# Kernel tuning notes

Measured on AMD Instinct MI355X. Metric: run time of the kernel, lower is better.

The kernel has to match this reference:

```python
import jax, jax.numpy as jnp
import numpy as np

NUM_CLASSES = 10
OUTPUT_DIM = 128
HIDDEN_DIM = 64


def setup_inputs() -> dict:
    key = jax.random.key(0)
    k1, k2, k3, k4, k5, k6 = jax.random.split(key, 6)
    B, S, F = 16, 4096, 512
    X_support = jax.random.normal(k1, (B, S, F), dtype=jnp.float32)
    y_support = jax.random.randint(k2, (B, S), 0, NUM_CLASSES, dtype=jnp.int32)
    # MLP params: Linear(6, HIDDEN) -> GELU -> Linear(HIDDEN, OUTPUT)
    w1 = jax.random.normal(k3, (6, HIDDEN_DIM), dtype=jnp.float32) * (1.0 / np.sqrt(6.0))
    b1 = jax.random.normal(k4, (HIDDEN_DIM,), dtype=jnp.float32) * 0.01
    w2 = jax.random.normal(k5, (HIDDEN_DIM, OUTPUT_DIM), dtype=jnp.float32) * (1.0 / np.sqrt(HIDDEN_DIM))
    b2 = jax.random.normal(k6, (OUTPUT_DIM,), dtype=jnp.float32) * 0.01
    return {"X_support": X_support, "y_support": y_support,
            "w1": w1, "b1": b1, "w2": w2, "b2": b2}


def _feature_target_stats(X, y):
    """Vectorized equivalent of FeatureTargetStatsEncoder per-(batch,feature) loops.
    X: [B, S, F] float, y: [B, S] int class labels. Returns stats [B, F, 6]."""
    B, S, F = X.shape
    missing_rate = jnp.isnan(X).astype(X.dtype).mean(axis=1)           # [B, F]
    Xc = jnp.nan_to_num(X, nan=0.0)
    gmean = Xc.mean(axis=1)                                            # [B, F]
    variance = Xc.var(axis=1)                                          # biased (unbiased=False)
    absX = jnp.abs(Xc)
    mean_abs = absX.mean(axis=1)
    max_abs = absX.max(axis=1)
    # unique_ratio: count distinct values per (b, f) via sort + diff
    xs = jnp.sort(Xc, axis=1)
    n_unique = 1.0 + (jnp.diff(xs, axis=1) != 0).astype(Xc.dtype).sum(axis=1)
    unique_ratio = n_unique / S
    # classification target score: between-class variance / overall variance
    onehot = jax.nn.one_hot(y, NUM_CLASSES, dtype=Xc.dtype)            # [B, S, C]
    counts = onehot.sum(axis=1)                                        # [B, C]
    csum = jnp.einsum('bsc,bsf->bcf', onehot, Xc)                      # [B, C, F]
    cmean = csum / jnp.maximum(counts, 1.0)[:, :, None]
    dev2 = (cmean - gmean[:, None, :]) ** 2
    between = (counts[:, :, None] * dev2).sum(axis=1) / jnp.maximum(counts.sum(axis=1), 1.0)[:, None]
    target_score = between / jnp.maximum(variance, 1e-6)
    stats = jnp.stack([target_score, missing_rate, unique_ratio,
                       variance, mean_abs, max_abs], axis=-1)          # [B, F, 6]
    return jnp.nan_to_num(stats, nan=0.0, posinf=0.0, neginf=0.0)


def reference(X_support, y_support, w1, b1, w2, b2):
    stats = _feature_target_stats(X_support, y_support)                # [B, F, 6]
    h = jax.nn.gelu(stats @ w1 + b1, approximate=False)               # exact GELU like nn.GELU()
    return h @ w2 + b2                                                 # [B, F, OUTPUT_DIM]
```

## Files before the change

### kernel.cpp

```cpp
#include <hip/hip_runtime.h>
#include <math.h>

#define NS 4096
#define NF 512
#define NB 16
#define NC 10
#define HSIZE 8192
#define HMASK 8191
#define HEMPTY 0xFFFFFFFFu
#define WS_XT_OFF 1024

__global__ void count_classes_kernel(const int* __restrict__ y, float* __restrict__ counts) {
    __shared__ int hist[NC];
    const int b = blockIdx.x;
    if (threadIdx.x < NC) hist[threadIdx.x] = 0;
    __syncthreads();
    for (int s = threadIdx.x; s < NS; s += blockDim.x)
        atomicAdd(&hist[y[b * NS + s]], 1);
    __syncthreads();
    if (threadIdx.x < NC) counts[b * NC + threadIdx.x] = (float)hist[threadIdx.x];
}

__device__ __forceinline__ float wave_reduce_add(float v) {
    #pragma unroll
    for (int off = 32; off > 0; off >>= 1) v += __shfl_down(v, off, 64);
    return v;
}
__device__ __forceinline__ float wave_reduce_max(float v) {
    #pragma unroll
    for (int off = 32; off > 0; off >>= 1) v = fmaxf(v, __shfl_down(v, off, 64));
    return v;
}

__launch_bounds__(256)
__global__ void transpose_kernel(const float* __restrict__ X, float* __restrict__ XT,
                                 const int* __restrict__ y, float* __restrict__ counts) {
    __shared__ float t[64][65];
    __shared__ int hist[NC];
    const int b  = blockIdx.x;
    const int s0 = blockIdx.y * 64;
    const int f0 = blockIdx.z * 64;
    const int tid = threadIdx.x;

    const int fi = (tid & 15) * 4;
    const int si = tid >> 4;
    const float* Xb = X + ((size_t)b * NS + s0) * NF + f0;
    #pragma unroll
    for (int i = 0; i < 4; i++) {
        const int s = si + 16 * i;
        const float4 v = *(const float4*)(Xb + (size_t)s * NF + fi);
        t[s][fi + 0] = v.x; t[s][fi + 1] = v.y;
        t[s][fi + 2] = v.z; t[s][fi + 3] = v.w;
    }
    __syncthreads();

    const int sj = (tid & 15) * 4;
    const int fj = tid >> 4;
    float* XTb = XT + ((size_t)b * NF + f0) * NS + s0;
    #pragma unroll
    for (int i = 0; i < 4; i++) {
        const int f = fj + 16 * i;
        float4 v;
        v.x = t[sj + 0][f]; v.y = t[sj + 1][f];
        v.z = t[sj + 2][f]; v.w = t[sj + 3][f];
        *(float4*)(XTb + (size_t)f * NS + sj) = v;
    }

    if (blockIdx.y == 0 && blockIdx.z == 0) {
        if (tid < NC) hist[tid] = 0;
        __syncthreads();
        const int4* yb = (const int4*)(y + (size_t)b * NS);
        #pragma unroll
        for (int i = 0; i < 4; i++) {
            const int4 v = yb[i * 256 + tid];
            atomicAdd(&hist[v.x], 1); atomicAdd(&hist[v.y], 1);
            atomicAdd(&hist[v.z], 1); atomicAdd(&hist[v.w], 1);
        }
        __syncthreads();
        if (tid < NC) counts[b * NC + tid] = (float)hist[tid];
    }
}

__launch_bounds__(512, 8)
__global__ void fused_stats_mlp_xt(const float* __restrict__ XT,
                                   const int* __restrict__ y,
                                   const float* __restrict__ counts,
                                   const float* __restrict__ w1,
                                   const float* __restrict__ b1,
                                   const float* __restrict__ w2,
                                   const float* __restrict__ b2,
                                   float* __restrict__ out) {
    __shared__ __align__(16) unsigned int hash[HSIZE];

    const int w = blockIdx.x;
    const int g = (w & 7) * 1024 + (w >> 3);
    const int b = g >> 9;
    const int f = g & (NF - 1);
    const int tid = threadIdx.x;
    const int wave = tid >> 6, lane = tid & 63;

    uint4* h4 = (uint4*)hash;
    const uint4 e4 = make_uint4(HEMPTY, HEMPTY, HEMPTY, HEMPTY);
    #pragma unroll
    for (int i = 0; i < HSIZE / 4 / 512; i++) h4[i * 512 + tid] = e4;
    __syncthreads();

    const float4* Xc4 = (const float4*)(XT + ((size_t)b * NF + f) * NS);
    const int4*   yp4 = (const int4*)(y + (size_t)b * NS);

    float sum = 0.f, sumsq = 0.f, sumabs = 0.f, maxabs = 0.f, nancnt = 0.f, uniq = 0.f;
    float csum[NC];
    #pragma unroll
    for (int c = 0; c < NC; c++) csum[c] = 0.f;

    float4 xv[2]; int4 yv[2];
    #pragma unroll
    for (int k = 0; k < 2; k++) {
        xv[k] = Xc4[k * 512 + tid];
        yv[k] = yp4[k * 512 + tid];
    }

    #pragma unroll
    for (int k = 0; k < 2; k++) {
        const float xe[4] = { xv[k].x, xv[k].y, xv[k].z, xv[k].w };
        const int   ye[4] = { yv[k].x, yv[k].y, yv[k].z, yv[k].w };
        #pragma unroll
        for (int j = 0; j < 4; j++) {
            float x = xe[j];
            if (x != x) { nancnt += 1.f; x = 0.f; }
            sum += x;
            sumsq = fmaf(x, x, sumsq);
            const float a = fabsf(x);
            sumabs += a;
            maxabs = fmaxf(maxabs, a);
            const int yc = ye[j];
            #pragma unroll
            for (int c = 0; c < NC; c++) csum[c] += (yc == c) ? x : 0.f;
            unsigned int pat = __float_as_uint(x);
            if (pat == 0x80000000u) pat = 0u;
            unsigned int slot = (pat * 2654435761u) >> 19;
            for (;;) {
                const unsigned int old = atomicCAS(&hash[slot], HEMPTY, pat);
                if (old == HEMPTY) { uniq += 1.f; break; }
                if (old == pat) break;
                slot = (slot + 1) & HMASK;
            }
        }
    }

    __syncthreads();

    float (*red)[16] = (float(*)[16])hash;
    float* stats_s   = (float*)hash + 128;
    float* h_s       = (float*)hash + 192;

    sum    = wave_reduce_add(sum);
    sumsq  = wave_reduce_add(sumsq);
    sumabs = wave_reduce_add(sumabs);
    nancnt = wave_reduce_add(nancnt);
    uniq   = wave_reduce_add(uniq);
    maxabs = wave_reduce_max(maxabs);
    #pragma unroll
    for (int c = 0; c < NC; c++) csum[c] = wave_reduce_add(csum[c]);

    if (lane == 0) {
        red[wave][0] = sum;    red[wave][1] = sumsq; red[wave][2] = sumabs;
        red[wave][3] = nancnt; red[wave][4] = uniq;  red[wave][5] = maxabs;
        #pragma unroll
        for (int c = 0; c < NC; c++) red[wave][6 + c] = csum[c];
    }
    __syncthreads();

    if (tid == 0) {
        float t[16];
        #pragma unroll
        for (int v = 0; v < 16; v++) t[v] = red[0][v];
        #pragma unroll
        for (int wv = 1; wv < 8; wv++) {
            #pragma unroll
            for (int v = 0; v < 16; v++) {
                if (v == 5) t[v] = fmaxf(t[v], red[wv][v]);
                else        t[v] += red[wv][v];
            }
        }
        const float invS = 1.f / (float)NS;
        const float gmean    = t[0] * invS;
        const float variance = fmaxf(t[1] * invS - gmean * gmean, 0.f);
        const float mean_abs = t[2] * invS;
        const float missing  = t[3] * invS;
        const float n_unique = t[4];
        const float max_abs  = t[5];
        float between = 0.f;
        #pragma unroll
        for (int c = 0; c < NC; c++) {
            const float cnt = counts[b * NC + c];
            const float cm  = t[6 + c] / fmaxf(cnt, 1.f);
            const float d   = cm - gmean;
            between += cnt * d * d;
        }
        between *= invS;
        const float target = between / fmaxf(variance, 1e-6f);
        float st[6] = { target, missing, n_unique * invS, variance, mean_abs, max_abs };
        #pragma unroll
        for (int i = 0; i < 6; i++) {
            float v = st[i];
            if (!(fabsf(v) < INFINITY)) v = 0.f;
            stats_s[i] = v;
        }
    }
    __syncthreads();

    if (tid < 64) {
        float z = b1[tid];
        #pragma unroll
        for (int i = 0; i < 6; i++) z = fmaf(stats_s[i], w1[i * 64 + tid], z);
        h_s[tid] = 0.5f * z * (1.f + erff(z * 0.70710678118654752440f));
    }
    __syncthreads();
    if (tid < 128) {
        float o = b2[tid];
        #pragma unroll
        for (int j = 0; j < 64; j++) o = fmaf(h_s[j], w2[j * 128 + tid], o);
        out[(size_t)g * 128 + tid] = o;
    }
}

__launch_bounds__(256)
__global__ void fused_stats_mlp_kernel(const float* __restrict__ X,
                                       const int* __restrict__ y,
                                       const float* __restrict__ counts,
                                       const float* __restrict__ w1,
                                       const float* __restrict__ b1,
                                       const float* __restrict__ w2,
                                       const float* __restrict__ b2,
                                       float* __restrict__ out) {
    __shared__ unsigned int hash[HSIZE];
    __shared__ float red[4][16];
    __shared__ float stats_s[6];
    __shared__ float h_s[64];

    const int w = blockIdx.x;
    const int g = (w & 7) * 1024 + (w >> 3);
    const int b = g >> 9;
    const int f = g & (NF - 1);
    const int tid = threadIdx.x;

    #pragma unroll
    for (int i = 0; i < HSIZE / 256; i++) hash[tid + i * 256] = HEMPTY;
    __syncthreads();

    const float* Xp = X + (size_t)b * NS * NF + f;
    const int*   yp = y + b * NS;

    float sum = 0.f, sumsq = 0.f, sumabs = 0.f, maxabs = 0.f, nancnt = 0.f, uniq = 0.f;
    float csum[NC];
    #pragma unroll
    for (int c = 0; c < NC; c++) csum[c] = 0.f;

    #pragma unroll
    for (int k0 = 0; k0 < 16; k0 += 8) {
        float xv[8]; int yv[8];
        #pragma unroll
        for (int k = 0; k < 8; k++) {
            const int s = (k0 + k) * 256 + tid;
            xv[k] = Xp[(size_t)s * NF];
            yv[k] = yp[s];
        }
        #pragma unroll
        for (int k = 0; k < 8; k++) {
            float x = xv[k];
            if (x != x) { nancnt += 1.f; x = 0.f; }
            sum += x;
            sumsq = fmaf(x, x, sumsq);
            const float a = fabsf(x);
            sumabs += a;
            maxabs = fmaxf(maxabs, a);
            const int yc = yv[k];
            #pragma unroll
            for (int c = 0; c < NC; c++) csum[c] += (yc == c) ? x : 0.f;
            unsigned int pat = __float_as_uint(x);
            if (pat == 0x80000000u) pat = 0u;
            unsigned int slot = (pat * 2654435761u) >> 19;
            for (;;) {
                const unsigned int old = atomicCAS(&hash[slot], HEMPTY, pat);
                if (old == HEMPTY) { uniq += 1.f; break; }
                if (old == pat) break;
                slot = (slot + 1) & HMASK;
            }
        }
    }

    sum    = wave_reduce_add(sum);
    sumsq  = wave_reduce_add(sumsq);
    sumabs = wave_reduce_add(sumabs);
    nancnt = wave_reduce_add(nancnt);
    uniq   = wave_reduce_add(uniq);
    maxabs = wave_reduce_max(maxabs);
    #pragma unroll
    for (int c = 0; c < NC; c++) csum[c] = wave_reduce_add(csum[c]);

    const int wave = tid >> 6, lane = tid & 63;
    if (lane == 0) {
        red[wave][0] = sum;    red[wave][1] = sumsq; red[wave][2] = sumabs;
        red[wave][3] = nancnt; red[wave][4] = uniq;  red[wave][5] = maxabs;
        #pragma unroll
        for (int c = 0; c < NC; c++) red[wave][6 + c] = csum[c];
    }
    __syncthreads();

    if (tid == 0) {
        float t[16];
        #pragma unroll
        for (int v = 0; v < 16; v++) t[v] = red[0][v];
        #pragma unroll
        for (int wv = 1; wv < 4; wv++) {
            #pragma unroll
            for (int v = 0; v < 16; v++) {
                if (v == 5) t[v] = fmaxf(t[v], red[wv][v]);
                else        t[v] += red[wv][v];
            }
        }
        const float invS = 1.f / (float)NS;
        const float gmean    = t[0] * invS;
        const float variance = fmaxf(t[1] * invS - gmean * gmean, 0.f);
        const float mean_abs = t[2] * invS;
        const float missing  = t[3] * invS;
        const float n_unique = t[4];
        const float max_abs  = t[5];
        float between = 0.f;
        #pragma unroll
        for (int c = 0; c < NC; c++) {
            const float cnt = counts[b * NC + c];
            const float cm  = t[6 + c] / fmaxf(cnt, 1.f);
            const float d   = cm - gmean;
            between += cnt * d * d;
        }
        between *= invS;
        const float target = between / fmaxf(variance, 1e-6f);
        float st[6] = { target, missing, n_unique * invS, variance, mean_abs, max_abs };
        #pragma unroll
        for (int i = 0; i < 6; i++) {
            float v = st[i];
            if (!(fabsf(v) < INFINITY)) v = 0.f;
            stats_s[i] = v;
        }
    }
    __syncthreads();

    if (tid < 64) {
        float z = b1[tid];
        #pragma unroll
        for (int i = 0; i < 6; i++) z = fmaf(stats_s[i], w1[i * 64 + tid], z);
        h_s[tid] = 0.5f * z * (1.f + erff(z * 0.70710678118654752440f));
    }
    __syncthreads();
    if (tid < 128) {
        float o = b2[tid];
        #pragma unroll
        for (int j = 0; j < 64; j++) o = fmaf(h_s[j], w2[j * 128 + tid], o);
        out[(size_t)g * 128 + tid] = o;
    }
}

extern "C" void kernel_launch(void* const* d_in, const int* in_sizes, int n_in,
                              void* d_out, int out_size, void* d_ws, size_t ws_size,
                              hipStream_t stream) {
    const float* X  = (const float*)d_in[0];
    const int*   y  = (const int*)d_in[1];
    const float* w1 = (const float*)d_in[2];
    const float* b1 = (const float*)d_in[3];
    const float* w2 = (const float*)d_in[4];
    const float* b2 = (const float*)d_in[5];
    float* out    = (float*)d_out;
    float* counts = (float*)d_ws;

    const size_t xt_bytes = (size_t)NB * NF * NS * sizeof(float);
    if (ws_size >= xt_bytes + WS_XT_OFF) {
        float* XT = (float*)((char*)d_ws + WS_XT_OFF);
        transpose_kernel<<<dim3(NB, NS / 64, NF / 64), 256, 0, stream>>>(X, XT, y, counts);
        fused_stats_mlp_xt<<<NB * NF, 512, 0, stream>>>(XT, y, counts, w1, b1, w2, b2, out);
    } else {
        count_classes_kernel<<<NB, 256, 0, stream>>>(y, counts);
        fused_stats_mlp_kernel<<<NB * NF, 256, 0, stream>>>(X, y, counts, w1, b1, w2, b2, out);
    }
}
```

Measured before the change: 388.7 us.

## Split stats and hash-unique work across wave groups with batched CAS

Splits the 512-thread block so waves 0-3 compute moments and class sums over 16 elements each, while waves 4-7 insert the same 16 elements into the shared-memory hash. Hash inserts are batched as 8 independent atomicCAS operations issued before any collision is resolved, so their LDS latency can overlap. The goal is to overlap ALU-heavy reduction with LDS-atomic-heavy unique counting and to raise memory-level parallelism. Each thread now handles twice as many elements, which raises register pressure, and X is loaded twice, by both wave groups.

```diff
diff --git a/kernel.cpp b/kernel.cpp
--- a/kernel.cpp
+++ b/kernel.cpp
@@ -30,6 +30,51 @@
     #pragma unroll
     for (int off = 32; off > 0; off >>= 1) v = fmaxf(v, __shfl_down(v, off, 64));
     return v;
+}
+
+__device__ __forceinline__ unsigned int pat_of(float x) {
+    if (x != x) x = 0.f;
+    unsigned int p = __float_as_uint(x);
+    return (p == 0x80000000u) ? 0u : p;
+}
+
+__device__ __forceinline__ float resolve1(unsigned int* hash,
+                                          unsigned int s, unsigned int p, unsigned int o) {
+    if (o == HEMPTY) return 1.f;
+    if (o == p)      return 0.f;
+    for (;;) {
+        s = (s + 1) & HMASK;
+        const unsigned int oo = atomicCAS(&hash[s], HEMPTY, p);
+        if (oo == HEMPTY) return 1.f;
+        if (oo == p)      return 0.f;
+    }
+}
+
+__device__ __forceinline__ float hash8(unsigned int* hash, const float4 u, const float4 v) {
+    const unsigned int p0 = pat_of(u.x), p1 = pat_of(u.y), p2 = pat_of(u.z), p3 = pat_of(u.w);
+    const unsigned int p4 = pat_of(v.x), p5 = pat_of(v.y), p6 = pat_of(v.z), p7 = pat_of(v.w);
+    const unsigned int s0 = (p0 * 2654435761u) >> 19, s1 = (p1 * 2654435761u) >> 19;
+    const unsigned int s2 = (p2 * 2654435761u) >> 19, s3 = (p3 * 2654435761u) >> 19;
+    const unsigned int s4 = (p4 * 2654435761u) >> 19, s5 = (p5 * 2654435761u) >> 19;
+    const unsigned int s6 = (p6 * 2654435761u) >> 19, s7 = (p7 * 2654435761u) >> 19;
+    const unsigned int o0 = atomicCAS(&hash[s0], HEMPTY, p0);
+    const unsigned int o1 = atomicCAS(&hash[s1], HEMPTY, p1);
+    const unsigned int o2 = atomicCAS(&hash[s2], HEMPTY, p2);
+    const unsigned int o3 = atomicCAS(&hash[s3], HEMPTY, p3);
+    const unsigned int o4 = atomicCAS(&hash[s4], HEMPTY, p4);
+    const unsigned int o5 = atomicCAS(&hash[s5], HEMPTY, p5);
+    const unsigned int o6 = atomicCAS(&hash[s6], HEMPTY, p6);
+    const unsigned int o7 = atomicCAS(&hash[s7], HEMPTY, p7);
+    float u8 = 0.f;
+    u8 += resolve1(hash, s0, p0, o0);
+    u8 += resolve1(hash, s1, p1, o1);
+    u8 += resolve1(hash, s2, p2, o2);
+    u8 += resolve1(hash, s3, p3, o3);
+    u8 += resolve1(hash, s4, p4, o4);
+    u8 += resolve1(hash, s5, p5, o5);
+    u8 += resolve1(hash, s6, p6, o6);
+    u8 += resolve1(hash, s7, p7, o7);
+    return u8;
 }
 
 __launch_bounds__(256)
@@ -113,39 +158,40 @@
     #pragma unroll
     for (int c = 0; c < NC; c++) csum[c] = 0.f;
 
-    float4 xv[2]; int4 yv[2];
-    #pragma unroll
-    for (int k = 0; k < 2; k++) {
-        xv[k] = Xc4[k * 512 + tid];
-        yv[k] = yp4[k * 512 + tid];
-    }
-
-    #pragma unroll
-    for (int k = 0; k < 2; k++) {
-        const float xe[4] = { xv[k].x, xv[k].y, xv[k].z, xv[k].w };
-        const int   ye[4] = { yv[k].x, yv[k].y, yv[k].z, yv[k].w };
-        #pragma unroll
-        for (int j = 0; j < 4; j++) {
-            float x = xe[j];
-            if (x != x) { nancnt += 1.f; x = 0.f; }
-            sum += x;
-            sumsq = fmaf(x, x, sumsq);
-            const float a = fabsf(x);
-            sumabs += a;
-            maxabs = fmaxf(maxabs, a);
-            const int yc = ye[j];
+    if (wave < 4) {
+        const int ts = tid;
+        float4 xv[4]; int4 yv[4];
+        #pragma unroll
+        for (int k = 0; k < 4; k++) {
+            xv[k] = Xc4[k * 256 + ts];
+            yv[k] = yp4[k * 256 + ts];
+        }
+        #pragma unroll
+        for (int k = 0; k < 4; k++) {
+            const float xe[4] = { xv[k].x, xv[k].y, xv[k].z, xv[k].w };
+            const int   ye[4] = { yv[k].x, yv[k].y, yv[k].z, yv[k].w };
             #pragma unroll
-            for (int c = 0; c < NC; c++) csum[c] += (yc == c) ? x : 0.f;
-            unsigned int pat = __float_as_uint(x);
-            if (pat == 0x80000000u) pat = 0u;
-            unsigned int slot = (pat * 2654435761u) >> 19;
-            for (;;) {
-                const unsigned int old = atomicCAS(&hash[slot], HEMPTY, pat);
-                if (old == HEMPTY) { uniq += 1.f; break; }
-                if (old == pat) break;
-                slot = (slot + 1) & HMASK;
+            for (int j = 0; j < 4; j++) {
+                float x = xe[j];
+                if (x != x) { nancnt += 1.f; x = 0.f; }
+                sum += x;
+                sumsq = fmaf(x, x, sumsq);
+                const float a = fabsf(x);
+                sumabs += a;
+                maxabs = fmaxf(maxabs, a);
+                const int yc = ye[j];
+                #pragma unroll
+                for (int c = 0; c < NC; c++) csum[c] += (yc == c) ? x : 0.f;
             }
         }
+    } else {
+        const int th = tid - 256;
+        const float4 xa = Xc4[th];
+        const float4 xb = Xc4[256 + th];
+        const float4 xc = Xc4[512 + th];
+        const float4 xd = Xc4[768 + th];
+        uniq += hash8(hash, xa, xb);
+        uniq += hash8(hash, xc, xd);
     }
 
     __syncthreads();
```

Result: faster. 373.1 us (-4.0%).
